# Kernel optimization log

Measured on AMD Instinct MI355X. Metric: run time of the kernel, lower is better.

## Reference

```python
import jax, jax.numpy as jnp
import numpy as np

D = 128
N = 50000
E = 600000


def setup_inputs() -> dict:
    key = jax.random.key(0)
    ks = jax.random.split(key, 6)
    x_a = jax.random.normal(ks[0], (N, D), dtype=jnp.float32)
    x_b = jax.random.normal(ks[1], (N, D), dtype=jnp.float32)
    ei_ab = jax.random.randint(ks[2], (2, E), 0, N)  # row0: src in 'a', row1: dst in 'b'
    ei_ba = jax.random.randint(ks[3], (2, E), 0, N)  # row0: src in 'b', row1: dst in 'a'
    scale = 1.0 / np.sqrt(D).astype(np.float32)
    # [layer, node_type(a,b), q/k/v, D, D]
    qkv_w = jax.random.normal(ks[4], (2, 2, 3, D, D), dtype=jnp.float32) * scale
    qkv_b = jnp.zeros((2, 2, 3, D), dtype=jnp.float32)
    # [layer, edge_type(ab,ba), D, D] -- bilinear attention weights
    edge_W = jax.random.normal(ks[5], (2, 2, D, D), dtype=jnp.float32) * scale
    return {"x_a": x_a, "x_b": x_b, "ei_ab": ei_ab, "ei_ba": ei_ba,
            "qkv_w": qkv_w, "qkv_b": qkv_b, "edge_W": edge_W}


def _edge_attend(q, k, v, W, src, dst, n_dst):
    """Bilinear per-edge attention + segment softmax over dst + scatter-add."""
    d = q.shape[-1]
    qW = q @ W                                   # [N_src, D] (node-level, cheap)
    s = jnp.sum(qW[src] * k[dst], axis=-1) / jnp.sqrt(jnp.asarray(d, q.dtype))  # [E]
    s = jax.nn.leaky_relu(s, negative_slope=0.01)
    m = jax.ops.segment_max(s, dst, num_segments=n_dst)      # per-dst max
    e = jnp.exp(s - m[dst])
    denom = jax.ops.segment_sum(e, dst, num_segments=n_dst)
    alpha = e / denom[dst]                                   # [E]
    return jax.ops.segment_sum(alpha[:, None] * v[src], dst, num_segments=n_dst)


def _layer(x_a, x_b, ei_ab, ei_ba, w, b, eW):
    # w: [2 types, 3, D, D]; b: [2, 3, D]; eW: [2 edge types, D, D]
    q_a, k_a, v_a = [x_a @ w[0, i] + b[0, i] for i in range(3)]
    q_b, k_b, v_b = [x_b @ w[1, i] + b[1, i] for i in range(3)]
    # edge type a->b: q/v from src type 'a', k from dst type 'b'
    out_b = _edge_attend(q_a, k_b, v_a, eW[0], ei_ab[0], ei_ab[1], x_b.shape[0])
    # edge type b->a: q/v from src type 'b', k from dst type 'a'
    out_a = _edge_attend(q_b, k_a, v_b, eW[1], ei_ba[0], ei_ba[1], x_a.shape[0])
    return out_a, out_b


def reference(x_a, x_b, ei_ab, ei_ba, qkv_w, qkv_b, edge_W):
    h_a, h_b = _layer(x_a, x_b, ei_ab, ei_ba, qkv_w[0], qkv_b[0], edge_W[0])
    h_a = jax.nn.relu(h_a)
    h_b = jax.nn.relu(h_b)
    o_a, o_b = _layer(h_a, h_b, ei_ab, ei_ba, qkv_w[1], qkv_b[1], edge_W[1])
    return o_a, o_b
```

## Files before the change

kernel.cpp:

```cpp
#include <hip/hip_runtime.h>
#include <math.h>

#define DD 128
#define CHUNK 8192
#define CAP 5120

typedef __attribute__((ext_vector_type(8))) short bf16x8;
typedef __attribute__((ext_vector_type(4))) float f32x4;

__device__ __forceinline__ ushort f2bf(float f) {
    union { float f; unsigned u; } v; v.f = f;
    unsigned r = v.u + 0x7fff + ((v.u >> 16) & 1);
    return (ushort)(r >> 16);
}

__device__ __forceinline__ float2 bfp(unsigned u) {
    union { unsigned x; float f; } a, b;
    a.x = u << 16;
    b.x = u & 0xffff0000u;
    return make_float2(a.f, b.f);
}

__global__ __launch_bounds__(256) void xcvt(const float* __restrict__ in,
                                            ushort* __restrict__ out, int n8)
{
    for (int i = blockIdx.x * 256 + threadIdx.x; i < n8; i += gridDim.x * 256) {
        float4 v0 = ((const float4*)in)[(size_t)i * 2];
        float4 v1 = ((const float4*)in)[(size_t)i * 2 + 1];
        bf16x8 h;
        h[0]=(short)f2bf(v0.x); h[1]=(short)f2bf(v0.y); h[2]=(short)f2bf(v0.z); h[3]=(short)f2bf(v0.w);
        h[4]=(short)f2bf(v1.x); h[5]=(short)f2bf(v1.y); h[6]=(short)f2bf(v1.z); h[7]=(short)f2bf(v1.w);
        *(bf16x8*)&out[(size_t)i * 8] = h;
    }
}

__global__ __launch_bounds__(256) void combine_all(const float* __restrict__ qkv_w,
                                                   const float* __restrict__ qkv_b,
                                                   const float* __restrict__ edge_W,
                                                   float* __restrict__ WC,
                                                   float* __restrict__ BCq)
{
    const int z = blockIdx.y;
    const int L = z >> 1, t = z & 1;
    const float* wq = qkv_w + (((size_t)L * 2 + t) * 3 + 0) * DD * DD;
    const float* bq = qkv_b + (((size_t)L * 2 + t) * 3 + 0) * DD;
    const float* We = edge_W + ((size_t)L * 2 + t) * DD * DD;
    float* Wz = WC + (size_t)z * DD * DD;
    float* Bz = BCq + (size_t)z * DD;

    const int tid = threadIdx.x;
    const int i = blockIdx.x * 2 + (tid >> 7);
    const int j = tid & 127;
    float sum = 0.f;
    for (int k = 0; k < DD; ++k) sum = fmaf(wq[i * DD + k], We[k * DD + j], sum);
    Wz[i * DD + j] = sum;
    if (blockIdx.x == 0 && tid < DD) {
        float s2 = 0.f;
        for (int k = 0; k < DD; ++k) s2 = fmaf(bq[k], We[k * DD + j], s2);
        Bz[j] = s2;
    }
}

__global__ __launch_bounds__(256) void pack_all(const float* __restrict__ qkv_w,
                                                const float* __restrict__ qkv_b,
                                                const float* __restrict__ WC,
                                                const float* __restrict__ BCq,
                                                ushort* __restrict__ W3P,
                                                float* __restrict__ B3)
{
    const int z = blockIdx.y;
    const int L = z >> 1, t = z & 1;
    const int ci = blockIdx.x * 256 + threadIdx.x;
    const int cb = ci >> 11;
    const int ct = (ci >> 8) & 7;
    const int ks = (ci >> 6) & 3;
    const int l  = ci & 63;
    const int c3 = cb * 128 + ct * 16 + (l & 15);
    const int k0 = ks * 32 + (l >> 4) * 8;

    const float* wv = qkv_w + (((size_t)L * 2 + t) * 3 + 2) * DD * DD;
    const float* wk = qkv_w + (((size_t)L * 2 + (t ^ 1)) * 3 + 1) * DD * DD;
    const float* src;
    int cc;
    if (c3 < 128)      { src = WC + (size_t)z * DD * DD; cc = c3; }
    else if (c3 < 256) { src = wv; cc = c3 - 128; }
    else               { src = wk; cc = c3 - 256; }

    ushort h[8];
    #pragma unroll
    for (int j = 0; j < 8; ++j) h[j] = f2bf(src[(size_t)(k0 + j) * DD + cc]);
    ushort* dst = W3P + (size_t)z * 6144 * 8 + (size_t)ci * 8;
    #pragma unroll
    for (int j = 0; j < 8; ++j) dst[j] = h[j];

    if (ci < 384) {
        float bv;
        if (ci < 128)      bv = BCq[(size_t)z * DD + ci];
        else if (ci < 256) bv = qkv_b[(((size_t)L * 2 + t) * 3 + 2) * DD + (ci - 128)];
        else               bv = qkv_b[(((size_t)L * 2 + (t ^ 1)) * 3 + 1) * DD + (ci - 256)];
        B3[(size_t)z * 384 + ci] = bv;
    }
}

template<bool RELU_IN>
__global__ __launch_bounds__(256, 4) void gemm_mfma(const ushort* __restrict__ Xsrc,
                                                    const ushort* __restrict__ Xdst,
                                                    const ushort* __restrict__ Bp,
                                                    const float* __restrict__ bias,
                                                    ushort* __restrict__ QV,
                                                    ushort* __restrict__ FK,
                                                    int N)
{
    const int by = blockIdx.y;
    const ushort* X = (by == 2) ? Xdst : Xsrc;
    const ushort* Bz = Bp + (size_t)by * 16384;
    const float* bz = bias + by * 128;
    ushort* outp   = (by == 2) ? FK : QV;
    const int stride = (by == 2) ? 128 : 256;
    const int off    = (by == 1) ? 128 : 0;

    const int wave = threadIdx.x >> 6;
    const int lane = threadIdx.x & 63;
    const int row0 = blockIdx.x * 64 + wave * 16;

    const int arow = row0 + (lane & 15);
    const bool aok = arow < N;
    const ushort* xr = X + (size_t)arow * DD + (lane >> 4) * 8;

    bf16x8 a[4];
    #pragma unroll
    for (int ks = 0; ks < 4; ++ks) {
        bf16x8 h = (bf16x8){0,0,0,0,0,0,0,0};
        if (aok) h = *(const bf16x8*)&xr[ks * 32];
        if (RELU_IN) {
            #pragma unroll
            for (int j = 0; j < 8; ++j)
                h[j] = (short)(((ushort)h[j] & 0x8000u) ? 0 : (ushort)h[j]);
        }
        a[ks] = h;
    }

    f32x4 acc[8];
    #pragma unroll
    for (int ct = 0; ct < 8; ++ct) {
        acc[ct] = (f32x4){0.f, 0.f, 0.f, 0.f};
        #pragma unroll
        for (int ks = 0; ks < 4; ++ks) {
            bf16x8 b = *(const bf16x8*)&Bz[(size_t)((ct * 4 + ks) * 64 + lane) * 8];
            acc[ct] = __builtin_amdgcn_mfma_f32_16x16x32_bf16(a[ks], b, acc[ct], 0, 0, 0);
        }
    }

    const int rbase = row0 + (lane >> 4) * 4;
    #pragma unroll
    for (int ct = 0; ct < 8; ++ct) {
        const int col = ct * 16 + (lane & 15);
        const float bv = bz[col];
        #pragma unroll
        for (int j = 0; j < 4; ++j) {
            const int rr = rbase + j;
            if (rr < N) outp[(size_t)rr * stride + off + col] = f2bf(acc[ct][j] + bv);
        }
    }
}

__global__ __launch_bounds__(256) void zero_ints(int* __restrict__ p, int n)
{
    int i = blockIdx.x * 256 + threadIdx.x;
    if (i < n) p[i] = 0;
}

__global__ __launch_bounds__(256) void bkt_hist(const int* __restrict__ dst0,
                                                const int* __restrict__ dst1,
                                                int* __restrict__ bcnt, int nE)
{
    const int t = blockIdx.y;
    const int* dst = t ? dst1 : dst0;
    __shared__ int h[256];
    h[threadIdx.x] = 0;
    __syncthreads();
    for (int e = blockIdx.x * 256 + threadIdx.x; e < nE; e += gridDim.x * 256)
        atomicAdd(&h[dst[e] >> 8], 1);
    __syncthreads();
    if (h[threadIdx.x]) atomicAdd(&bcnt[t * 256 + threadIdx.x], h[threadIdx.x]);
}

__global__ __launch_bounds__(64) void bkt_scan(const int* __restrict__ bcnt,
                                               int* __restrict__ bbase,
                                               int* __restrict__ bcur,
                                               int* __restrict__ offs0,
                                               int* __restrict__ offs1, int N, int nE)
{
    if (threadIdx.x < 2) {
        int t = threadIdx.x;
        int run = 0;
        for (int i = 0; i < 256; ++i) {
            int v = bcnt[t * 256 + i];
            bbase[t * 256 + i] = run;
            bcur[t * 256 + i] = run;
            run += v;
        }
        if (t == 0) offs0[N] = nE; else offs1[N] = nE;
    }
}

__global__ __launch_bounds__(256) void bkt_part(const int* __restrict__ src0,
                                                const int* __restrict__ dst0,
                                                const int* __restrict__ src1,
                                                const int* __restrict__ dst1,
                                                int* __restrict__ bcur,
                                                unsigned* __restrict__ stage0,
                                                unsigned* __restrict__ stage1,
                                                int nE, int nbkt)
{
    const int t = blockIdx.y;
    const int* src = t ? src1 : src0;
    const int* dst = t ? dst1 : dst0;
    unsigned* stage = t ? stage1 : stage0;
    int* bc = bcur + t * 256;

    __shared__ unsigned ebuf[CHUNK];
    __shared__ int cnt[256], loff[256], cur[256], resv[256];

    const int tid  = threadIdx.x;
    const int e0   = blockIdx.x * CHUNK;
    const int ecnt = min(CHUNK, nE - e0);

    cnt[tid] = 0;
    __syncthreads();

    unsigned pk[CHUNK / 256];
    #pragma unroll
    for (int i = 0; i < CHUNK / 256; ++i) {
        const int le = i * 256 + tid;
        unsigned p = 0xFFFFFFFFu;
        if (le < ecnt) {
            int d = dst[e0 + le], s = src[e0 + le];
            p = ((unsigned)(d >> 8) << 24) | ((unsigned)(d & 255) << 16) | (unsigned)s;
            atomicAdd(&cnt[d >> 8], 1);
        }
        pk[i] = p;
    }
    __syncthreads();

    int v = cnt[tid];
    loff[tid] = v;
    __syncthreads();
    for (int off = 1; off < 256; off <<= 1) {
        int a = (tid >= off) ? loff[tid - off] : 0;
        __syncthreads();
        loff[tid] += a;
        __syncthreads();
    }
    int excl = loff[tid] - v;
    __syncthreads();
    loff[tid] = excl;
    cur[tid]  = excl;
    __syncthreads();

    #pragma unroll
    for (int i = 0; i < CHUNK / 256; ++i) {
        unsigned p = pk[i];
        if (p != 0xFFFFFFFFu) {
            int b = p >> 24;
            int pos = atomicAdd(&cur[b], 1);
            ebuf[pos] = p;
        }
    }
    __syncthreads();

    if (tid < nbkt && cnt[tid] > 0) resv[tid] = atomicAdd(&bc[tid], cnt[tid]);
    __syncthreads();

    const int wv = tid >> 6, ln = tid & 63;
    for (int b = wv; b < nbkt; b += 4) {
        const int c = cnt[b];
        if (c == 0) continue;
        const int lo = loff[b];
        const int rb = resv[b];
        for (int i = ln; i < c; i += 64) stage[rb + i] = ebuf[lo + i];
    }
}

__global__ __launch_bounds__(256) void bkt_fill(const unsigned* __restrict__ stage0,
                                                const unsigned* __restrict__ stage1,
                                                const int* __restrict__ bcnt,
                                                const int* __restrict__ bbase,
                                                int* __restrict__ offs0,
                                                int* __restrict__ offs1,
                                                int* __restrict__ col0,
                                                int* __restrict__ col1, int N)
{
    const int b = blockIdx.x, t = blockIdx.y;
    const unsigned* stage = t ? stage1 : stage0;
    int* offs = t ? offs1 : offs0;
    int* col  = t ? col1 : col0;
    const int base = bbase[t * 256 + b];
    int cb = bcnt[t * 256 + b];
    if (cb > CAP) cb = CAP;

    __shared__ unsigned ebuf[CAP];
    __shared__ int colbuf[CAP];
    __shared__ int dcnt[256], doff[256], dcur[256];

    const int tid = threadIdx.x;
    dcnt[tid] = 0;
    __syncthreads();

    for (int i = tid; i < cb; i += 256) {
        unsigned p = stage[base + i];
        ebuf[i] = p;
        atomicAdd(&dcnt[(p >> 16) & 255], 1);
    }
    __syncthreads();

    int v = dcnt[tid];
    doff[tid] = v;
    __syncthreads();
    for (int off = 1; off < 256; off <<= 1) {
        int a = (tid >= off) ? doff[tid - off] : 0;
        __syncthreads();
        doff[tid] += a;
        __syncthreads();
    }
    int excl = doff[tid] - v;
    dcur[tid] = excl;
    const int node = (b << 8) + tid;
    if (node < N) offs[node] = base + excl;
    __syncthreads();

    for (int i = tid; i < cb; i += 256) {
        unsigned p = ebuf[i];
        int pos = atomicAdd(&dcur[(p >> 16) & 255], 1);
        colbuf[pos] = (int)(p & 0xFFFFu);
    }
    __syncthreads();

    for (int i = tid; i < cb; i += 256) col[base + i] = colbuf[i];
}

template<bool BF16_OUT>
__global__ __launch_bounds__(256) void attn_gather(const ushort* __restrict__ QV,
                                                   const ushort* __restrict__ K,
                                                   const int* __restrict__ offs,
                                                   const int* __restrict__ col,
                                                   void* __restrict__ outv, int n)
{
    const int wid  = (blockIdx.x * 256 + threadIdx.x) >> 6;
    const int lane = threadIdx.x & 63;
    if (wid >= n) return;
    const int li = lane & 15;
    const int g  = lane >> 4;

    const int beg = offs[wid], end = offs[wid + 1];

    uint4 ku = ((const uint4*)(K + (size_t)wid * DD))[li];
    float kf[8];
    {
        float2 t;
        t = bfp(ku.x); kf[0]=t.x; kf[1]=t.y;
        t = bfp(ku.y); kf[2]=t.x; kf[3]=t.y;
        t = bfp(ku.z); kf[4]=t.x; kf[5]=t.y;
        t = bfp(ku.w); kf[6]=t.x; kf[7]=t.y;
    }

    float m = -__builtin_inff();
    float den = 0.f;
    float acc[8] = {0.f,0.f,0.f,0.f,0.f,0.f,0.f,0.f};

    int p = beg + g;
    uint4 qn = make_uint4(0,0,0,0), vn = make_uint4(0,0,0,0);
    if (p < end) {
        const ushort* row = QV + (size_t)col[p] * 256;
        qn = ((const uint4*)row)[li];
        vn = ((const uint4*)(row + 128))[li];
    }

    while (p < end) {
        uint4 qu = qn, vu = vn;
        const int pn = p + 4;
        if (pn < end) {
            const ushort* row = QV + (size_t)col[pn] * 256;
            qn = ((const uint4*)row)[li];
            vn = ((const uint4*)(row + 128))[li];
        }
        float2 t;
        float d;
        t = bfp(qu.x); d  = t.x*kf[0] + t.y*kf[1];
        t = bfp(qu.y); d += t.x*kf[2] + t.y*kf[3];
        t = bfp(qu.z); d += t.x*kf[4] + t.y*kf[5];
        t = bfp(qu.w); d += t.x*kf[6] + t.y*kf[7];
        d += __shfl_xor(d, 1);
        d += __shfl_xor(d, 2);
        d += __shfl_xor(d, 4);
        d += __shfl_xor(d, 8);
        float sc = d * 0.08838834764831845f;
        sc = sc > 0.f ? sc : 0.01f * sc;
        float nm = fmaxf(m, sc);
        float f  = __expf(m - nm);
        float pe = __expf(sc - nm);
        den = den * f + pe;
        float2 v0 = bfp(vu.x), v1 = bfp(vu.y), v2 = bfp(vu.z), v3 = bfp(vu.w);
        acc[0] = acc[0]*f + pe*v0.x;  acc[1] = acc[1]*f + pe*v0.y;
        acc[2] = acc[2]*f + pe*v1.x;  acc[3] = acc[3]*f + pe*v1.y;
        acc[4] = acc[4]*f + pe*v2.x;  acc[5] = acc[5]*f + pe*v2.y;
        acc[6] = acc[6]*f + pe*v3.x;  acc[7] = acc[7]*f + pe*v3.y;
        m = nm;
        p = pn;
    }

    float m1 = fmaxf(m, __shfl_xor(m, 16));
    float m2 = fmaxf(m1, __shfl_xor(m1, 32));
    float f = (den > 0.f) ? __expf(m - m2) : 0.f;
    den *= f;
    den += __shfl_xor(den, 16);
    den += __shfl_xor(den, 32);
    #pragma unroll
    for (int j = 0; j < 8; ++j) {
        acc[j] *= f;
        acc[j] += __shfl_xor(acc[j], 16);
        acc[j] += __shfl_xor(acc[j], 32);
    }
    if (g == 0) {
        const float inv = den > 0.f ? 1.f / den : 0.f;
        if (BF16_OUT) {
            ushort* o = (ushort*)outv + (size_t)wid * DD + li * 8;
            bf16x8 h;
            #pragma unroll
            for (int j = 0; j < 8; ++j) h[j] = (short)f2bf(acc[j] * inv);
            *(bf16x8*)o = h;
        } else {
            float* o = (float*)outv + (size_t)wid * DD + li * 8;
            *(float4*)o       = make_float4(acc[0]*inv, acc[1]*inv, acc[2]*inv, acc[3]*inv);
            *(float4*)(o + 4) = make_float4(acc[4]*inv, acc[5]*inv, acc[6]*inv, acc[7]*inv);
        }
    }
}

extern "C" void kernel_launch(void* const* d_in, const int* in_sizes, int n_in,
                              void* d_out, int out_size, void* d_ws, size_t ws_size,
                              hipStream_t stream)
{
    const float* x_a    = (const float*)d_in[0];
    const float* x_b    = (const float*)d_in[1];
    const int*   ei_ab  = (const int*)d_in[2];
    const int*   ei_ba  = (const int*)d_in[3];
    const float* qkv_w  = (const float*)d_in[4];
    const float* qkv_b  = (const float*)d_in[5];
    const float* edge_W = (const float*)d_in[6];
    float* out = (float*)d_out;

    const int N = in_sizes[0] / DD;
    const int E = in_sizes[2] / 2;
    const int nbkt = (N + 255) >> 8;

    float* ws = (float*)d_ws;
    float* WC  = ws;
    float* BCq = WC + 4 * DD * DD;
    float* B3  = BCq + 4 * DD;
    ushort* W3P = (ushort*)(B3 + 4 * 384);
    ushort* XA = W3P + (size_t)4 * 6144 * 8;
    ushort* XB = XA + (size_t)N * DD;
    ushort* HA = XB + (size_t)N * DD;
    ushort* HB = HA + (size_t)N * DD;
    ushort* QV = HB + (size_t)N * DD;
    ushort* FK = QV + (size_t)N * 256;
    int* ip      = (int*)(FK + (size_t)N * DD);
    int* bcnt    = ip;
    int* bbase   = bcnt + 512;
    int* bcur    = bbase + 512;
    int* offs_ab = bcur + 512;
    int* offs_ba = offs_ab + (N + 1);
    int* col_ab  = offs_ba + (N + 1);
    int* col_ba  = col_ab + E;
    unsigned* stage0 = (unsigned*)(col_ba + E);
    unsigned* stage1 = stage0 + E;

    {
        dim3 g1(64, 4);
        combine_all<<<g1, 256, 0, stream>>>(qkv_w, qkv_b, edge_W, WC, BCq);
        dim3 g2(24, 4);
        pack_all<<<g2, 256, 0, stream>>>(qkv_w, qkv_b, WC, BCq, W3P, B3);
        const int n8 = N * DD / 8;
        xcvt<<<2048, 256, 0, stream>>>(x_a, XA, n8);
        xcvt<<<2048, 256, 0, stream>>>(x_b, XB, n8);
    }

    const int* s_ab = ei_ab;  const int* d_ab = ei_ab + E;
    const int* s_ba = ei_ba;  const int* d_ba = ei_ba + E;
    {
        zero_ints<<<2, 256, 0, stream>>>(bcnt, 512);
        dim3 hg(128, 2);
        bkt_hist<<<hg, 256, 0, stream>>>(d_ab, d_ba, bcnt, E);
        bkt_scan<<<1, 64, 0, stream>>>(bcnt, bbase, bcur, offs_ab, offs_ba, N, E);
        dim3 pg((E + CHUNK - 1) / CHUNK, 2);
        bkt_part<<<pg, 256, 0, stream>>>(s_ab, d_ab, s_ba, d_ba, bcur,
                                         stage0, stage1, E, nbkt);
        dim3 fg(nbkt, 2);
        bkt_fill<<<fg, 256, 0, stream>>>(stage0, stage1, bcnt, bbase,
                                         offs_ab, offs_ba, col_ab, col_ba, N);
    }

    const dim3 gemm_grid((N + 63) / 64, 3);
    const int ag_grid = (N + 3) / 4;

    auto attend = [&](int z, const ushort* Xsrc, const ushort* Xdst, bool relu_in,
                      const int* offs, const int* col, void* outbuf, bool bf16_out) {
        const ushort* Bp = W3P + (size_t)z * 6144 * 8;
        const float* bz  = B3 + (size_t)z * 384;
        if (relu_in)
            gemm_mfma<true ><<<gemm_grid, 256, 0, stream>>>(Xsrc, Xdst, Bp, bz, QV, FK, N);
        else
            gemm_mfma<false><<<gemm_grid, 256, 0, stream>>>(Xsrc, Xdst, Bp, bz, QV, FK, N);
        if (bf16_out)
            attn_gather<true ><<<ag_grid, 256, 0, stream>>>(QV, FK, offs, col, outbuf, N);
        else
            attn_gather<false><<<ag_grid, 256, 0, stream>>>(QV, FK, offs, col, outbuf, N);
    };

    attend(0, XA, XB, false, offs_ab, col_ab, HB, true);
    attend(1, XB, XA, false, offs_ba, col_ba, HA, true);
    float* o_a = out;
    float* o_b = out + (size_t)N * DD;
    attend(2, HA, HB, true, offs_ab, col_ab, o_b, false);
    attend(3, HB, HA, true, offs_ba, col_ba, o_a, false);
}
```

Measured before the change: 381.1 us.

## Fuse input bf16 conversion into GEMM and batch per-layer projections per node type

The separate fp32-to-bf16 conversion kernels for x_a and x_b are removed, and the layer-0 GEMM now reads fp32 inputs and converts them in registers. Each GEMM block now computes all three projections (qW, v, k) for its own node type, reusing the loaded A tile three times. One launch per layer covers both node types instead of two launches per layer. The k projection is re-indexed to the block's own type, with separate output buffers per type. The aim is fewer launches, less intermediate traffic, and better reuse of A, at the cost of a longer per-block loop and more workspace.

```diff
diff --git a/kernel.cpp b/kernel.cpp
--- a/kernel.cpp
+++ b/kernel.cpp
@@ -19,19 +19,6 @@
     a.x = u << 16;
     b.x = u & 0xffff0000u;
     return make_float2(a.f, b.f);
-}
-
-__global__ __launch_bounds__(256) void xcvt(const float* __restrict__ in,
-                                            ushort* __restrict__ out, int n8)
-{
-    for (int i = blockIdx.x * 256 + threadIdx.x; i < n8; i += gridDim.x * 256) {
-        float4 v0 = ((const float4*)in)[(size_t)i * 2];
-        float4 v1 = ((const float4*)in)[(size_t)i * 2 + 1];
-        bf16x8 h;
-        h[0]=(short)f2bf(v0.x); h[1]=(short)f2bf(v0.y); h[2]=(short)f2bf(v0.z); h[3]=(short)f2bf(v0.w);
-        h[4]=(short)f2bf(v1.x); h[5]=(short)f2bf(v1.y); h[6]=(short)f2bf(v1.z); h[7]=(short)f2bf(v1.w);
-        *(bf16x8*)&out[(size_t)i * 8] = h;
-    }
 }
 
 __global__ __launch_bounds__(256) void combine_all(const float* __restrict__ qkv_w,
@@ -79,7 +66,7 @@
     const int k0 = ks * 32 + (l >> 4) * 8;
 
     const float* wv = qkv_w + (((size_t)L * 2 + t) * 3 + 2) * DD * DD;
-    const float* wk = qkv_w + (((size_t)L * 2 + (t ^ 1)) * 3 + 1) * DD * DD;
+    const float* wk = qkv_w + (((size_t)L * 2 + t) * 3 + 1) * DD * DD;
     const float* src;
     int cc;
     if (c3 < 128)      { src = WC + (size_t)z * DD * DD; cc = c3; }
@@ -97,69 +84,94 @@
         float bv;
         if (ci < 128)      bv = BCq[(size_t)z * DD + ci];
         else if (ci < 256) bv = qkv_b[(((size_t)L * 2 + t) * 3 + 2) * DD + (ci - 128)];
-        else               bv = qkv_b[(((size_t)L * 2 + (t ^ 1)) * 3 + 1) * DD + (ci - 256)];
+        else               bv = qkv_b[(((size_t)L * 2 + t) * 3 + 1) * DD + (ci - 256)];
         B3[(size_t)z * 384 + ci] = bv;
     }
 }
 
-template<bool RELU_IN>
-__global__ __launch_bounds__(256, 4) void gemm_mfma(const ushort* __restrict__ Xsrc,
-                                                    const ushort* __restrict__ Xdst,
-                                                    const ushort* __restrict__ Bp,
-                                                    const float* __restrict__ bias,
-                                                    ushort* __restrict__ QV,
-                                                    ushort* __restrict__ FK,
+template<bool F32_IN, bool RELU_IN>
+__global__ __launch_bounds__(256, 4) void gemm_mfma(const void* __restrict__ Xav,
+                                                    const void* __restrict__ Xbv,
+                                                    const ushort* __restrict__ WpL,
+                                                    const float* __restrict__ bL,
+                                                    ushort* __restrict__ QVa,
+                                                    ushort* __restrict__ FKa,
+                                                    ushort* __restrict__ QVb,
+                                                    ushort* __restrict__ FKb,
                                                     int N)
 {
-    const int by = blockIdx.y;
-    const ushort* X = (by == 2) ? Xdst : Xsrc;
-    const ushort* Bz = Bp + (size_t)by * 16384;
-    const float* bz = bias + by * 128;
-    ushort* outp   = (by == 2) ? FK : QV;
-    const int stride = (by == 2) ? 128 : 256;
-    const int off    = (by == 1) ? 128 : 0;
+    const int t = blockIdx.y;
+    ushort* QV = t ? QVb : QVa;
+    ushort* FK = t ? FKb : FKa;
+    const ushort* Wz = WpL + (size_t)t * 49152;
+    const float* bz0 = bL + (size_t)t * 384;
 
     const int wave = threadIdx.x >> 6;
     const int lane = threadIdx.x & 63;
     const int row0 = blockIdx.x * 64 + wave * 16;
-
     const int arow = row0 + (lane & 15);
     const bool aok = arow < N;
-    const ushort* xr = X + (size_t)arow * DD + (lane >> 4) * 8;
+    const int kcol = (lane >> 4) * 8;
 
     bf16x8 a[4];
-    #pragma unroll
-    for (int ks = 0; ks < 4; ++ks) {
-        bf16x8 h = (bf16x8){0,0,0,0,0,0,0,0};
-        if (aok) h = *(const bf16x8*)&xr[ks * 32];
-        if (RELU_IN) {
-            #pragma unroll
-            for (int j = 0; j < 8; ++j)
-                h[j] = (short)(((ushort)h[j] & 0x8000u) ? 0 : (ushort)h[j]);
-        }
-        a[ks] = h;
-    }
-
-    f32x4 acc[8];
-    #pragma unroll
-    for (int ct = 0; ct < 8; ++ct) {
-        acc[ct] = (f32x4){0.f, 0.f, 0.f, 0.f};
+    if (F32_IN) {
+        const float* X = (const float*)(t ? Xbv : Xav);
+        const float* xr = X + (size_t)arow * DD + kcol;
         #pragma unroll
         for (int ks = 0; ks < 4; ++ks) {
-            bf16x8 b = *(const bf16x8*)&Bz[(size_t)((ct * 4 + ks) * 64 + lane) * 8];
-            acc[ct] = __builtin_amdgcn_mfma_f32_16x16x32_bf16(a[ks], b, acc[ct], 0, 0, 0);
+            bf16x8 h = (bf16x8){0,0,0,0,0,0,0,0};
+            if (aok) {
+                float4 v0 = *(const float4*)&xr[ks * 32];
+                float4 v1 = *(const float4*)&xr[ks * 32 + 4];
+                h[0]=(short)f2bf(v0.x); h[1]=(short)f2bf(v0.y); h[2]=(short)f2bf(v0.z); h[3]=(short)f2bf(v0.w);
+                h[4]=(short)f2bf(v1.x); h[5]=(short)f2bf(v1.y); h[6]=(short)f2bf(v1.z); h[7]=(short)f2bf(v1.w);
+            }
+            a[ks] = h;
+        }
+    } else {
+        const ushort* X = (const ushort*)(t ? Xbv : Xav);
+        const ushort* xr = X + (size_t)arow * DD + kcol;
+        #pragma unroll
+        for (int ks = 0; ks < 4; ++ks) {
+            bf16x8 h = (bf16x8){0,0,0,0,0,0,0,0};
+            if (aok) h = *(const bf16x8*)&xr[ks * 32];
+            if (RELU_IN) {
+                #pragma unroll
+                for (int j = 0; j < 8; ++j)
+                    h[j] = (short)(((ushort)h[j] & 0x8000u) ? 0 : (ushort)h[j]);
+            }
+            a[ks] = h;
         }
     }
 
     const int rbase = row0 + (lane >> 4) * 4;
     #pragma unroll
-    for (int ct = 0; ct < 8; ++ct) {
-        const int col = ct * 16 + (lane & 15);
-        const float bv = bz[col];
+    for (int p = 0; p < 3; ++p) {
+        const ushort* Bp = Wz + (size_t)p * 16384;
+        const float* bz = bz0 + p * 128;
+        ushort* outp   = (p == 2) ? FK : QV;
+        const int stride = (p == 2) ? 128 : 256;
+        const int off    = (p == 1) ? 128 : 0;
+
+        f32x4 acc[8];
         #pragma unroll
-        for (int j = 0; j < 4; ++j) {
-            const int rr = rbase + j;
-            if (rr < N) outp[(size_t)rr * stride + off + col] = f2bf(acc[ct][j] + bv);
+        for (int ct = 0; ct < 8; ++ct) {
+            acc[ct] = (f32x4){0.f, 0.f, 0.f, 0.f};
+            #pragma unroll
+            for (int ks = 0; ks < 4; ++ks) {
+                bf16x8 b = *(const bf16x8*)&Bp[(size_t)((ct * 4 + ks) * 64 + lane) * 8];
+                acc[ct] = __builtin_amdgcn_mfma_f32_16x16x32_bf16(a[ks], b, acc[ct], 0, 0, 0);
+            }
+        }
+        #pragma unroll
+        for (int ct = 0; ct < 8; ++ct) {
+            const int col = ct * 16 + (lane & 15);
+            const float bv = bz[col];
+            #pragma unroll
+            for (int j = 0; j < 4; ++j) {
+                const int rr = rbase + j;
+                if (rr < N) outp[(size_t)rr * stride + off + col] = f2bf(acc[ct][j] + bv);
+            }
         }
     }
 }
@@ -459,13 +471,13 @@
     float* BCq = WC + 4 * DD * DD;
     float* B3  = BCq + 4 * DD;
     ushort* W3P = (ushort*)(B3 + 4 * 384);
-    ushort* XA = W3P + (size_t)4 * 6144 * 8;
-    ushort* XB = XA + (size_t)N * DD;
-    ushort* HA = XB + (size_t)N * DD;
-    ushort* HB = HA + (size_t)N * DD;
-    ushort* QV = HB + (size_t)N * DD;
-    ushort* FK = QV + (size_t)N * 256;
-    int* ip      = (int*)(FK + (size_t)N * DD);
+    ushort* HA  = W3P + (size_t)4 * 49152;
+    ushort* HB  = HA + (size_t)N * DD;
+    ushort* QVa = HB + (size_t)N * DD;
+    ushort* QVb = QVa + (size_t)N * 256;
+    ushort* FKa = QVb + (size_t)N * 256;
+    ushort* FKb = FKa + (size_t)N * DD;
+    int* ip      = (int*)(FKb + (size_t)N * DD);
     int* bcnt    = ip;
     int* bbase   = bcnt + 512;
     int* bcur    = bbase + 512;
@@ -481,9 +493,6 @@
         combine_all<<<g1, 256, 0, stream>>>(qkv_w, qkv_b, edge_W, WC, BCq);
         dim3 g2(24, 4);
         pack_all<<<g2, 256, 0, stream>>>(qkv_w, qkv_b, WC, BCq, W3P, B3);
-        const int n8 = N * DD / 8;
-        xcvt<<<2048, 256, 0, stream>>>(x_a, XA, n8);
-        xcvt<<<2048, 256, 0, stream>>>(x_b, XB, n8);
     }
 
     const int* s_ab = ei_ab;  const int* d_ab = ei_ab + E;
@@ -501,27 +510,18 @@
                                          offs_ab, offs_ba, col_ab, col_ba, N);
     }
 
-    const dim3 gemm_grid((N + 63) / 64, 3);
+    const dim3 gemm_grid((N + 63) / 64, 2);
     const int ag_grid = (N + 3) / 4;
 
-    auto attend = [&](int z, const ushort* Xsrc, const ushort* Xdst, bool relu_in,
-                      const int* offs, const int* col, void* outbuf, bool bf16_out) {
-        const ushort* Bp = W3P + (size_t)z * 6144 * 8;
-        const float* bz  = B3 + (size_t)z * 384;
-        if (relu_in)
-            gemm_mfma<true ><<<gemm_grid, 256, 0, stream>>>(Xsrc, Xdst, Bp, bz, QV, FK, N);
-        else
-            gemm_mfma<false><<<gemm_grid, 256, 0, stream>>>(Xsrc, Xdst, Bp, bz, QV, FK, N);
-        if (bf16_out)
-            attn_gather<true ><<<ag_grid, 256, 0, stream>>>(QV, FK, offs, col, outbuf, N);
-        else
-            attn_gather<false><<<ag_grid, 256, 0, stream>>>(QV, FK, offs, col, outbuf, N);
-    };
-
-    attend(0, XA, XB, false, offs_ab, col_ab, HB, true);
-    attend(1, XB, XA, false, offs_ba, col_ba, HA, true);
+    gemm_mfma<true, false><<<gemm_grid, 256, 0, stream>>>(
+        x_a, x_b, W3P, B3, QVa, FKa, QVb, FKb, N);
+    attn_gather<true><<<ag_grid, 256, 0, stream>>>(QVa, FKb, offs_ab, col_ab, HB, N);
+    attn_gather<true><<<ag_grid, 256, 0, stream>>>(QVb, FKa, offs_ba, col_ba, HA, N);
+
     float* o_a = out;
     float* o_b = out + (size_t)N * DD;
-    attend(2, HA, HB, true, offs_ab, col_ab, o_b, false);
-    attend(3, HB, HA, true, offs_ba, col_ba, o_a, false);
-}
+    gemm_mfma<false, true><<<gemm_grid, 256, 0, stream>>>(
+        HA, HB, W3P + (size_t)2 * 49152, B3 + 2 * 384, QVa, FKa, QVb, FKb, N);
+    attn_gather<false><<<ag_grid, 256, 0, stream>>>(QVa, FKb, offs_ab, col_ab, o_b, N);
+    attn_gather<false><<<ag_grid, 256, 0, stream>>>(QVb, FKa, offs_ba, col_ba, o_a, N);
+}
```

Result: faster. 352.8 us (-7.4%).
